# Optimization experiments

Hardware: AMD Instinct MI355X
Metric: run time of the kernel (lower is better)

## Reference

```python
import jax, jax.numpy as jnp
import numpy as np

K = 512
DIM = 64


def setup_inputs() -> dict:
    key = jax.random.key(0)
    kx, ke = jax.random.split(key)
    x = jax.random.normal(kx, (64, 64, 32, 32), dtype=jnp.float32)  # (b, d, h, w)
    codebook = jax.random.normal(ke, (K, DIM), dtype=jnp.float32)  # nn.Embedding weight
    return {"x": x, "codebook": codebook}


def reference(x, codebook):
    b, d, h, w = x.shape
    # (b, d, h*w) -> (b, h*w, d)
    flat = jnp.transpose(x.reshape(b, d, h * w), (0, 2, 1))  # (b, n, d)
    x2 = jnp.sum(flat * flat, axis=-1, keepdims=True)              # (b, n, 1)
    e2 = jnp.sum(codebook * codebook, axis=-1)                     # (k,)
    xe = jnp.einsum('bnd,kd->bnk', flat, codebook)                 # (b, n, k)
    dist = x2 - 2.0 * xe + e2                                      # (b, n, k)
    idx = jnp.argmin(dist, axis=-1)                                # (b, n)
    quant = codebook[idx]                                          # (b, n, d) gather
    # straight-through estimator
    quant_st = flat + jax.lax.stop_gradient(quant - flat)
    out = jnp.transpose(quant_st, (0, 2, 1)).reshape(b, d, h, w)
    return out
```

## Files before the change

### kernel.cpp

```cpp
#include <hip/hip_runtime.h>

#define KCODES 512
#define DIM    64
#define NVEC   65536
#define TAU    0.05f

typedef __attribute__((ext_vector_type(8))) short   short8;
typedef __attribute__((ext_vector_type(4))) float   f32x4;

static __device__ __forceinline__ unsigned f2bfu(float f) {
    unsigned u = __builtin_bit_cast(unsigned, f);
    u += 0x7fffu + ((u >> 16) & 1u);
    return u >> 16;
}

static __device__ __forceinline__ void glds16(const unsigned short* g,
                                              unsigned short* l) {
    __builtin_amdgcn_global_load_lds(
        (const __attribute__((address_space(1))) unsigned int*)g,
        (__attribute__((address_space(3))) unsigned int*)l, 16, 0, 0);
}

__global__ void prep_kernel(const float* __restrict__ cb,
                            unsigned short* __restrict__ cbt,
                            float* __restrict__ e2q) {
    if (blockIdx.x < 128) {
        const int g   = blockIdx.x * 64 + threadIdx.x;
        const int s   = g >> 10;
        const int rem = g & 1023;
        const int h   = rem >> 9;
        const int qd  = (rem >> 6) & 7;
        const int cl  = rem & 63;
        const float* src = cb + (size_t)(s * 64 + cl) * DIM + qd * 8;
        short8 v;
#pragma unroll
        for (int j = 0; j < 8; ++j) {
            float f = src[j];
            unsigned u = __builtin_bit_cast(unsigned, f);
            if (h == 0) {
                v[j] = (short)(u >> 16);
            } else {
                float hi = __builtin_bit_cast(float, u & 0xFFFF0000u);
                v[j] = (short)f2bfu(f - hi);
            }
        }
        *(short8*)(cbt + (size_t)g * 8) = v;
    } else {
        const int k = blockIdx.x - 128;
        float v = cb[k * DIM + threadIdx.x];
        double p = (double)v * (double)v;
#pragma unroll
        for (int off = 32; off > 0; off >>= 1) p += __shfl_down(p, off, 64);
        if (threadIdx.x == 0) e2q[k] = (float)(0.5 * p + 256.0);
    }
}

__launch_bounds__(256, 4)
__global__ void vq_main(const float* __restrict__ x,
                        const float* __restrict__ cb,
                        const unsigned short* __restrict__ cbt,
                        const float* __restrict__ e2q,
                        float* __restrict__ out) {
    __shared__ __align__(16) unsigned short sA[2][8192];
    __shared__ float sE2[KCODES];

    unsigned short* sB = sA[1];
    unsigned char* scr = (unsigned char*)sA[0];
    float* s_pf1 = (float*)(scr);
    float* s_pf2 = (float*)(scr + 512);
    int*   s_pi1 = (int*)(scr + 1024);
    int*   s_pi2 = (int*)(scr + 1536);
    int*   s_i1  = (int*)(scr + 2048);
    int*   s_i2  = (int*)(scr + 2304);
    int*   s_flag= (int*)(scr + 2560);
    int*   s_win = (int*)(scr + 2816);

    const int tid  = threadIdx.x;
    const int wave = tid >> 6;
    const int lane = tid & 63;
    const int quad = lane >> 4;
    const int l16  = lane & 15;
    const int wr   = wave >> 1;
    const int wc   = wave & 1;

    const int v0    = blockIdx.x * 64;
    const int b     = v0 >> 10;
    const int nbase = v0 & 1023;
    const float* xb = x + (size_t)b * 65536;

#pragma unroll
    for (int r = 0; r < 4; ++r)
        glds16(cbt + (size_t)(r * 256 + wave * 64 + lane) * 8,
               sA[0] + (size_t)(r * 256 + wave * 64) * 8);

    {
        const int n_g = nbase + wave * 16 + l16;
#pragma unroll
        for (int ko = 0; ko < 2; ++ko) {
            short8 bh, bl;
#pragma unroll
            for (int j = 0; j < 8; ++j) {
                const int d = quad * 8 + j + ko * 32;
                float f = -xb[(size_t)d * 1024 + n_g];
                unsigned u = __builtin_bit_cast(unsigned, f);
                float hi = __builtin_bit_cast(float, u & 0xFFFF0000u);
                bh[j] = (short)(u >> 16);
                bl[j] = (short)f2bfu(f - hi);
            }
            *(short8*)(sB + (size_t)(wave * 256 +       ko * 64 + lane) * 8) = bh;
            *(short8*)(sB + (size_t)(wave * 256 + 128 + ko * 64 + lane) * 8) = bl;
        }
    }

    if (tid < 128) *(f32x4*)(sE2 + tid * 4) = *(const f32x4*)(e2q + tid * 4);
    __syncthreads();

    short8 Bh[2][2], Bl[2][2];
#pragma unroll
    for (int t = 0; t < 2; ++t) {
        const int tile = 2 * wr + t;
#pragma unroll
        for (int ko = 0; ko < 2; ++ko) {
            Bh[t][ko] = *(const short8*)(sB + (size_t)(tile * 256 +       ko * 64 + lane) * 8);
            Bl[t][ko] = *(const short8*)(sB + (size_t)(tile * 256 + 128 + ko * 64 + lane) * 8);
        }
    }
    __syncthreads();

    float f1[2], f2_[2];
    int   i1[2], i2_[2];
#pragma unroll
    for (int t = 0; t < 2; ++t) {
        f1[t] = 1e30f; f2_[t] = 1e30f; i1[t] = 0; i2_[t] = 0;
    }

#pragma unroll 1
    for (int s = 0; s < 8; ++s) {
        if (s < 7) {
#pragma unroll
            for (int r = 0; r < 4; ++r)
                glds16(cbt + (size_t)((s + 1) * 1024 + r * 256 + wave * 64 + lane) * 8,
                       sA[(s + 1) & 1] + (size_t)(r * 256 + wave * 64) * 8);
        }

        const unsigned short* buf = sA[s & 1];
#pragma unroll
        for (int st = 0; st < 2; ++st) {
            const int roff  = quad * 64 + wc * 32 + st * 16 + l16;
            short8 A00 = *(const short8*)(buf + (size_t)(      roff) * 8);
            short8 A01 = *(const short8*)(buf + (size_t)(256 + roff) * 8);
            short8 A10 = *(const short8*)(buf + (size_t)(512 + roff) * 8);
            short8 A11 = *(const short8*)(buf + (size_t)(768 + roff) * 8);
            const int cbase = s * 64 + wc * 32 + st * 16;
            const int idb   = cbase + quad * 4;
            f32x4 e2v = *(const f32x4*)(sE2 + idb);

#pragma unroll
            for (int t = 0; t < 2; ++t) {
                f32x4 acc = e2v;
                acc = __builtin_amdgcn_mfma_f32_16x16x32_bf16(A00, Bh[t][0], acc, 0, 0, 0);
                acc = __builtin_amdgcn_mfma_f32_16x16x32_bf16(A01, Bh[t][1], acc, 0, 0, 0);
                acc = __builtin_amdgcn_mfma_f32_16x16x32_bf16(A00, Bl[t][0], acc, 0, 0, 0);
                acc = __builtin_amdgcn_mfma_f32_16x16x32_bf16(A01, Bl[t][1], acc, 0, 0, 0);
                acc = __builtin_amdgcn_mfma_f32_16x16x32_bf16(A10, Bh[t][0], acc, 0, 0, 0);
                acc = __builtin_amdgcn_mfma_f32_16x16x32_bf16(A11, Bh[t][1], acc, 0, 0, 0);

#pragma unroll
                for (int r = 0; r < 4; ++r) {
                    float dd = acc[r];
                    int   id = idb + r;
                    bool  c1 = dd < f1[t];
                    bool  c2 = dd < f2_[t];
                    i2_[t] = c1 ? i1[t] : (c2 ? id : i2_[t]);
                    f2_[t] = fminf(fmaxf(f1[t], dd), f2_[t]);
                    i1[t]  = c1 ? id : i1[t];
                    f1[t]  = fminf(f1[t], dd);
                }
            }
        }
        __syncthreads();
    }

#pragma unroll
    for (int t = 0; t < 2; ++t) {
        float F1 = f1[t], F2 = f2_[t];
        int   I1 = i1[t], I2 = i2_[t];
#pragma unroll
        for (int delta = 16; delta <= 32; delta <<= 1) {
            float of1 = __shfl_xor(F1, delta, 64);
            int   oi1 = __shfl_xor(I1, delta, 64);
            float of2 = __shfl_xor(F2, delta, 64);
            int   oi2 = __shfl_xor(I2, delta, 64);
            bool o1_first = (of1 < F1) || (of1 == F1 && oi1 < I1);
            if (o1_first) {
                bool keep = (F1 < of2) || (F1 == of2 && I1 < oi2);
                F2 = keep ? F1 : of2;
                I2 = keep ? I1 : oi2;
                F1 = of1; I1 = oi1;
            } else {
                bool o1_second = (of1 < F2) || (of1 == F2 && oi1 < I2);
                if (o1_second) { F2 = of1; I2 = oi1; }
            }
        }
        if (quad == 0) {
            const int v = wr * 32 + t * 16 + l16;
            s_pf1[v * 2 + wc] = F1;
            s_pf2[v * 2 + wc] = F2;
            s_pi1[v * 2 + wc] = I1;
            s_pi2[v * 2 + wc] = I2;
        }
    }
    __syncthreads();

    if (tid < 64) {
        const int v = tid;
        float F1 = s_pf1[v * 2 + 0], F2 = s_pf2[v * 2 + 0];
        int   I1 = s_pi1[v * 2 + 0], I2 = s_pi2[v * 2 + 0];
        {
            float of1 = s_pf1[v * 2 + 1], of2 = s_pf2[v * 2 + 1];
            int   oi1 = s_pi1[v * 2 + 1], oi2 = s_pi2[v * 2 + 1];
            bool o1_first = (of1 < F1) || (of1 == F1 && oi1 < I1);
            if (o1_first) {
                bool keep = (F1 < of2) || (F1 == of2 && I1 < oi2);
                F2 = keep ? F1 : of2;
                I2 = keep ? I1 : oi2;
                F1 = of1; I1 = oi1;
            } else {
                bool o1_second = (of1 < F2) || (of1 == F2 && oi1 < I2);
                if (o1_second) { F2 = of1; I2 = oi1; }
            }
        }
        s_win[v]  = I1;
        s_i1[v]   = I1;
        s_i2[v]   = I2;
        s_flag[v] = (F2 - F1) < TAU;
    }
    __syncthreads();

    {
        const int vec = tid >> 2, sub = tid & 3;
        if (s_flag[vec]) {
            const int i1c = s_i1[vec], i2c = s_i2[vec];
            const float* xr = xb + nbase + vec;
            const float* r1 = cb + (size_t)i1c * DIM;
            const float* r2 = cb + (size_t)i2c * DIM;
            double D1 = 0.0, D2 = 0.0;
#pragma unroll 4
            for (int i = 0; i < 16; ++i) {
                const int d = sub + 4 * i;
                double xd = (double)xr[(size_t)d * 1024];
                double t1 = xd - (double)r1[d]; D1 += t1 * t1;
                double t2 = xd - (double)r2[d]; D2 += t2 * t2;
            }
            D1 += __shfl_down(D1, 2, 64); D1 += __shfl_down(D1, 1, 64);
            D2 += __shfl_down(D2, 2, 64); D2 += __shfl_down(D2, 1, 64);
            if (sub == 0) {
                if (D2 < D1 || (D2 == D1 && i2c < i1c)) s_win[vec] = i2c;
            }
        }
    }
    __syncthreads();

    {
        const int n    = tid & 63;
        const int dgrp = tid >> 6;
        const float4* crow = (const float4*)(cb + (size_t)s_win[n] * DIM);
        float* op = out + (size_t)b * 65536 + nbase + n;
#pragma unroll
        for (int i = 0; i < 4; ++i) {
            const int d0 = dgrp * 16 + i * 4;
            float4 val = crow[d0 >> 2];
            op[(size_t)(d0 + 0) * 1024] = val.x;
            op[(size_t)(d0 + 1) * 1024] = val.y;
            op[(size_t)(d0 + 2) * 1024] = val.z;
            op[(size_t)(d0 + 3) * 1024] = val.w;
        }
    }
}

extern "C" void kernel_launch(void* const* d_in, const int* in_sizes, int n_in,
                              void* d_out, int out_size, void* d_ws, size_t ws_size,
                              hipStream_t stream) {
    const float* x  = (const float*)d_in[0];
    const float* cb = (const float*)d_in[1];
    float* out = (float*)d_out;

    unsigned short* cbt = (unsigned short*)d_ws;
    float*          e2q = (float*)(cbt + 8192 * 8);

    prep_kernel<<<640, 64, 0, stream>>>(cb, cbt, e2q);
    vq_main<<<NVEC / 64, 256, 0, stream>>>(x, cb, cbt, e2q, out);
}
```

Before: 94.59 us.

## Give each wave a private double-buffered codebook stream, removing block barriers

Replaces the block-shared double-buffered codebook tile loop, which issued a __syncthreads every stage, with per-wave private LDS buffers. Each wave streams only its own code-column half through the buffers with a depth-2 prefetch, gated by explicit vmcnt waits. The inter-wave barrier disappears from the main loop, but waves sharing a column half now each load the same codebook data separately, which doubles global-to-LDS traffic. Correctness depends on the hand-written vmcnt counting matching the number of outstanding loads, and the main loop issues no LDS-specific wait after those loads land.

```diff
diff --git a/kernel.cpp b/kernel.cpp
--- a/kernel.cpp
+++ b/kernel.cpp
@@ -61,11 +61,11 @@
                         const unsigned short* __restrict__ cbt,
                         const float* __restrict__ e2q,
                         float* __restrict__ out) {
-    __shared__ __align__(16) unsigned short sA[2][8192];
+    __shared__ __align__(16) unsigned short sPriv[4][4096];
     __shared__ float sE2[KCODES];
 
-    unsigned short* sB = sA[1];
-    unsigned char* scr = (unsigned char*)sA[0];
+    unsigned short* sB = &sPriv[0][0];
+    unsigned char* scr = (unsigned char*)&sPriv[0][0];
     float* s_pf1 = (float*)(scr);
     float* s_pf2 = (float*)(scr + 512);
     int*   s_pi1 = (int*)(scr + 1024);
@@ -88,11 +88,6 @@
     const int nbase = v0 & 1023;
     const float* xb = x + (size_t)b * 65536;
 
-#pragma unroll
-    for (int r = 0; r < 4; ++r)
-        glds16(cbt + (size_t)(r * 256 + wave * 64 + lane) * 8,
-               sA[0] + (size_t)(r * 256 + wave * 64) * 8);
-
     {
         const int n_g = nbase + wave * 16 + l16;
 #pragma unroll
@@ -127,59 +122,66 @@
     }
     __syncthreads();
 
-    float f1[2], f2_[2];
-    int   i1[2], i2_[2];
-#pragma unroll
-    for (int t = 0; t < 2; ++t) {
-        f1[t] = 1e30f; f2_[t] = 1e30f; i1[t] = 0; i2_[t] = 0;
-    }
+    unsigned short* wbuf = &sPriv[wave][0];
+    const int glb = (lane >> 4) * 64 + (lane & 15);
+
+#define STAGE(sp_)                                                            \
+    {                                                                         \
+        const int sb_ = wc * 4096 + ((sp_) >> 2) * 1024 + ((sp_) & 3) * 16 + glb; \
+        unsigned short* d_ = wbuf + ((sp_) & 1) * 2048;                       \
+        _Pragma("unroll")                                                     \
+        for (int i_ = 0; i_ < 4; ++i_)                                        \
+            glds16(cbt + (size_t)(sb_ + i_ * 256) * 8, d_ + i_ * 512);        \
+    }
+
+    STAGE(0)
+    STAGE(1)
+
+    float f1[2] = {1e30f, 1e30f}, f2_[2] = {1e30f, 1e30f};
+    int   i1[2] = {0, 0},         i2_[2] = {0, 0};
 
 #pragma unroll 1
-    for (int s = 0; s < 8; ++s) {
-        if (s < 7) {
-#pragma unroll
-            for (int r = 0; r < 4; ++r)
-                glds16(cbt + (size_t)((s + 1) * 1024 + r * 256 + wave * 64 + lane) * 8,
-                       sA[(s + 1) & 1] + (size_t)(r * 256 + wave * 64) * 8);
-        }
-
-        const unsigned short* buf = sA[s & 1];
-#pragma unroll
-        for (int st = 0; st < 2; ++st) {
-            const int roff  = quad * 64 + wc * 32 + st * 16 + l16;
-            short8 A00 = *(const short8*)(buf + (size_t)(      roff) * 8);
-            short8 A01 = *(const short8*)(buf + (size_t)(256 + roff) * 8);
-            short8 A10 = *(const short8*)(buf + (size_t)(512 + roff) * 8);
-            short8 A11 = *(const short8*)(buf + (size_t)(768 + roff) * 8);
-            const int cbase = s * 64 + wc * 32 + st * 16;
-            const int idb   = cbase + quad * 4;
-            f32x4 e2v = *(const f32x4*)(sE2 + idb);
-
-#pragma unroll
-            for (int t = 0; t < 2; ++t) {
-                f32x4 acc = e2v;
-                acc = __builtin_amdgcn_mfma_f32_16x16x32_bf16(A00, Bh[t][0], acc, 0, 0, 0);
-                acc = __builtin_amdgcn_mfma_f32_16x16x32_bf16(A01, Bh[t][1], acc, 0, 0, 0);
-                acc = __builtin_amdgcn_mfma_f32_16x16x32_bf16(A00, Bl[t][0], acc, 0, 0, 0);
-                acc = __builtin_amdgcn_mfma_f32_16x16x32_bf16(A01, Bl[t][1], acc, 0, 0, 0);
-                acc = __builtin_amdgcn_mfma_f32_16x16x32_bf16(A10, Bh[t][0], acc, 0, 0, 0);
-                acc = __builtin_amdgcn_mfma_f32_16x16x32_bf16(A11, Bh[t][1], acc, 0, 0, 0);
-
-#pragma unroll
-                for (int r = 0; r < 4; ++r) {
-                    float dd = acc[r];
-                    int   id = idb + r;
-                    bool  c1 = dd < f1[t];
-                    bool  c2 = dd < f2_[t];
-                    i2_[t] = c1 ? i1[t] : (c2 ? id : i2_[t]);
-                    f2_[t] = fminf(fmaxf(f1[t], dd), f2_[t]);
-                    i1[t]  = c1 ? id : i1[t];
-                    f1[t]  = fminf(f1[t], dd);
-                }
-            }
-        }
-        __syncthreads();
-    }
+    for (int sp = 0; sp < 16; ++sp) {
+        if (sp < 15) { asm volatile("s_waitcnt vmcnt(4)" ::: "memory"); }
+        else         { asm volatile("s_waitcnt vmcnt(0)" ::: "memory"); }
+
+        const unsigned short* buf = wbuf + (sp & 1) * 2048;
+        short8 A00 = *(const short8*)(buf + (size_t)(       lane) * 8);
+        short8 A01 = *(const short8*)(buf + (size_t)( 64 + lane) * 8);
+        short8 A10 = *(const short8*)(buf + (size_t)(128 + lane) * 8);
+        short8 A11 = *(const short8*)(buf + (size_t)(192 + lane) * 8);
+        const int cbase = wc * 256 + sp * 16;
+        const int idb   = cbase + quad * 4;
+        f32x4 e2v = *(const f32x4*)(sE2 + idb);
+
+#pragma unroll
+        for (int t = 0; t < 2; ++t) {
+            f32x4 acc = e2v;
+            acc = __builtin_amdgcn_mfma_f32_16x16x32_bf16(A00, Bh[t][0], acc, 0, 0, 0);
+            acc = __builtin_amdgcn_mfma_f32_16x16x32_bf16(A01, Bh[t][1], acc, 0, 0, 0);
+            acc = __builtin_amdgcn_mfma_f32_16x16x32_bf16(A00, Bl[t][0], acc, 0, 0, 0);
+            acc = __builtin_amdgcn_mfma_f32_16x16x32_bf16(A01, Bl[t][1], acc, 0, 0, 0);
+            acc = __builtin_amdgcn_mfma_f32_16x16x32_bf16(A10, Bh[t][0], acc, 0, 0, 0);
+            acc = __builtin_amdgcn_mfma_f32_16x16x32_bf16(A11, Bh[t][1], acc, 0, 0, 0);
+
+#pragma unroll
+            for (int r = 0; r < 4; ++r) {
+                float dd = acc[r];
+                int   id = idb + r;
+                bool  c1 = dd < f1[t];
+                bool  c2 = dd < f2_[t];
+                i2_[t] = c1 ? i1[t] : (c2 ? id : i2_[t]);
+                f2_[t] = fminf(fmaxf(f1[t], dd), f2_[t]);
+                i1[t]  = c1 ? id : i1[t];
+                f1[t]  = fminf(f1[t], dd);
+            }
+        }
+
+        __builtin_amdgcn_sched_barrier(0);
+        if (sp < 14) STAGE(sp + 2)
+    }
+
+    __syncthreads();
 
 #pragma unroll
     for (int t = 0; t < 2; ++t) {
```

After: 95.57 us. Within noise of the previous version (+1.0%).
